# Kernel tuning notes

Measured on AMD Instinct MI355X. Metric: run time of the kernel, lower is better.

Reference implementation:

```python
import jax, jax.numpy as jnp
import numpy as np

B, S, DIM, BITS, HEXPERTS = 4, 4096, 2048, 32, 4


def setup_inputs() -> dict:
    key = jax.random.key(0)
    ks = jax.random.split(key, 6)
    scale = 1.0 / np.sqrt(DIM)
    return {
        "x": jax.random.normal(ks[0], (B, S, DIM), dtype=jnp.float32),
        "A1_w": jax.random.normal(ks[1], (BITS, DIM), dtype=jnp.float32) * scale,
        "A1_b": jax.random.normal(ks[2], (BITS,), dtype=jnp.float32) * 0.01,
        "emb": jax.random.normal(ks[3], (BITS, DIM), dtype=jnp.float32),
        "aggr_w": jax.random.normal(ks[4], (HEXPERTS,), dtype=jnp.float32) * 0.5,
        "aggr_b": jax.random.normal(ks[5], (1,), dtype=jnp.float32) * 0.01,
    }


def reference(x, A1_w, A1_b, emb, aggr_w, aggr_b):
    # Router: small linear [B,S,DIM] -> [B,S,BITS], softmax over bits.
    logits = jnp.einsum("bsd,kd->bsk", x, A1_w) + A1_b
    h_c = jax.nn.softmax(logits, axis=-1)
    # Top-k expert selection (k = Hexperts = 4), sorted descending like torch.topk.
    v, i = jax.lax.top_k(h_c, HEXPERTS)  # v,i: [B,S,4]
    # Gather expert embeddings: [B,S,4,DIM]
    h_emb = emb[i]
    # Scale by gate values and combine across experts with the 4->1 linear.
    # expert_aggr(h_emb.transpose(-2,-1)) == sum_e v[...,e]*h_emb[...,e,:]*w[e] + b
    out = jnp.einsum("bse,bsed,e->bsd", v, h_emb, aggr_w) + aggr_b[0]
    # Residual multiply (dropout p=0 -> identity).
    return x * out
```

## Files before the change

kernel.cpp:

```cpp
#include <hip/hip_runtime.h>


#define NTOK 16384
#define DIMV 2048

__global__ __launch_bounds__(512, 4) void fused_moe(
    const float* __restrict__ x,
    const float* __restrict__ A1w,
    const float* __restrict__ A1b,
    const float* __restrict__ emb,
    const float* __restrict__ aggw,
    const float* __restrict__ aggb,
    float* __restrict__ out)
{
    __shared__ float smem[9216];
    __shared__ float g_lds[256];

    const int tid  = threadIdx.x;
    const int wid  = tid >> 6;
    const int lane = tid & 63;
    const int tg   = lane & 7;
    const int kg   = lane >> 3;
    const int tok0 = blockIdx.x << 5;
    const int d0   = wid << 8;

    float* xs  = smem + wid * 1152;
    float* wsx = xs + 576;

    const int srow = lane >> 2;
    const int scol = (lane & 3) << 2;

    const float* xg0 = x   + (size_t)(tok0 + srow)      * DIMV + d0 + scol;
    const float* xg1 = x   + (size_t)(tok0 + srow + 16) * DIMV + d0 + scol;
    const float* wg0 = A1w + (size_t)(srow)             * DIMV + d0 + scol;
    const float* wg1 = A1w + (size_t)(srow + 16)        * DIMV + d0 + scol;

    float2 acc[4][4];
    #pragma unroll
    for (int i = 0; i < 4; ++i)
        #pragma unroll
        for (int j = 0; j < 4; ++j) acc[i][j] = make_float2(0.f, 0.f);

    float4 px0 = *(const float4*)(xg0);
    float4 px1 = *(const float4*)(xg1);
    float4 pw0 = *(const float4*)(wg0);
    float4 pw1 = *(const float4*)(wg1);

    for (int c = 0; c < 16; ++c) {
        {
            float* a = xs  + srow * 18 + scol;
            float* b = xs  + (srow + 16) * 18 + scol;
            float* d = wsx + srow * 18 + scol;
            float* e = wsx + (srow + 16) * 18 + scol;
            *(float2*)(a)     = make_float2(px0.x, px0.y);
            *(float2*)(a + 2) = make_float2(px0.z, px0.w);
            *(float2*)(b)     = make_float2(px1.x, px1.y);
            *(float2*)(b + 2) = make_float2(px1.z, px1.w);
            *(float2*)(d)     = make_float2(pw0.x, pw0.y);
            *(float2*)(d + 2) = make_float2(pw0.z, pw0.w);
            *(float2*)(e)     = make_float2(pw1.x, pw1.y);
            *(float2*)(e + 2) = make_float2(pw1.z, pw1.w);
        }
        {
            const int cn = (c + 1) & 15;
            px0 = *(const float4*)(xg0 + cn * 16);
            px1 = *(const float4*)(xg1 + cn * 16);
            pw0 = *(const float4*)(wg0 + cn * 16);
            pw1 = *(const float4*)(wg1 + cn * 16);
        }
        #pragma unroll
        for (int dd = 0; dd < 16; dd += 2) {
            float2 xv[4], wv[4];
            #pragma unroll
            for (int i = 0; i < 4; ++i)
                xv[i] = *(const float2*)&xs[(4 * tg + i) * 18 + dd];
            #pragma unroll
            for (int j = 0; j < 4; ++j)
                wv[j] = *(const float2*)&wsx[(4 * kg + j) * 18 + dd];
            #pragma unroll
            for (int i = 0; i < 4; ++i)
                #pragma unroll
                for (int j = 0; j < 4; ++j) {
                    acc[i][j].x = fmaf(xv[i].x, wv[j].x, acc[i][j].x);
                    acc[i][j].y = fmaf(xv[i].y, wv[j].y, acc[i][j].y);
                }
        }
    }

    __syncthreads();
    float* red = smem;
    #pragma unroll
    for (int i = 0; i < 4; ++i)
        #pragma unroll
        for (int j = 0; j < 4; ++j)
            red[(4 * tg + i) * 260 + ((4 * kg + j) << 3) + wid] =
                acc[i][j].x + acc[i][j].y;
    __syncthreads();

    if (tid < 32) {
        const int t = tid;
        float l[32];
        #pragma unroll
        for (int k = 0; k < 32; ++k) {
            float4 p0 = *(const float4*)&red[t * 260 + (k << 3)];
            float4 p1 = *(const float4*)&red[t * 260 + (k << 3) + 4];
            l[k] = ((p0.x + p0.y) + (p0.z + p0.w))
                 + ((p1.x + p1.y) + (p1.z + p1.w)) + A1b[k];
        }
        float m = l[0];
        #pragma unroll
        for (int k = 1; k < 32; ++k) m = fmaxf(m, l[k]);
        float s = 0.f;
        #pragma unroll
        for (int k = 0; k < 32; ++k) { l[k] = expf(l[k] - m); s += l[k]; }
        const float inv = 1.0f / s;

        unsigned used = 0u;
        #pragma unroll
        for (int e = 0; e < 4; ++e) {
            float best = -1.f; int bi = 0;
            #pragma unroll
            for (int k = 0; k < 32; ++k) {
                bool ok = !((used >> k) & 1u) && (l[k] > best);
                best = ok ? l[k] : best;
                bi   = ok ? k    : bi;
            }
            used |= (1u << bi);
            g_lds[t * 8 + e]     = best * inv * aggw[e];
            g_lds[t * 8 + 4 + e] = __uint_as_float((unsigned)bi);
        }
    }
    __syncthreads();

    const int tt  = tid >> 4;
    const int l16 = tid & 15;
    const float4 g = *(const float4*)&g_lds[tt * 8];
    const unsigned i0 = __float_as_uint(g_lds[tt * 8 + 4]);
    const unsigned i1 = __float_as_uint(g_lds[tt * 8 + 5]);
    const unsigned i2 = __float_as_uint(g_lds[tt * 8 + 6]);
    const unsigned i3 = __float_as_uint(g_lds[tt * 8 + 7]);
    const float bb = aggb[0];
    const size_t base = (size_t)(tok0 + tt) * DIMV;

    #pragma unroll 4
    for (int it = 0; it < 32; ++it) {
        const int d = (l16 << 2) + (it << 6);
        const float4 xv = *(const float4*)&x[base + d];
        const float4 e0 = *(const float4*)&emb[(size_t)i0 * DIMV + d];
        const float4 e1 = *(const float4*)&emb[(size_t)i1 * DIMV + d];
        const float4 e2 = *(const float4*)&emb[(size_t)i2 * DIMV + d];
        const float4 e3 = *(const float4*)&emb[(size_t)i3 * DIMV + d];
        float4 a, o;
        a.x = fmaf(g.x, e0.x, fmaf(g.y, e1.x, fmaf(g.z, e2.x, fmaf(g.w, e3.x, bb))));
        a.y = fmaf(g.x, e0.y, fmaf(g.y, e1.y, fmaf(g.z, e2.y, fmaf(g.w, e3.y, bb))));
        a.z = fmaf(g.x, e0.z, fmaf(g.y, e1.z, fmaf(g.z, e2.z, fmaf(g.w, e3.z, bb))));
        a.w = fmaf(g.x, e0.w, fmaf(g.y, e1.w, fmaf(g.z, e2.w, fmaf(g.w, e3.w, bb))));
        o.x = xv.x * a.x; o.y = xv.y * a.y; o.z = xv.z * a.z; o.w = xv.w * a.w;
        *(float4*)&out[base + d] = o;
    }
}

extern "C" void kernel_launch(void* const* d_in, const int* in_sizes, int n_in,
                              void* d_out, int out_size, void* d_ws, size_t ws_size,
                              hipStream_t stream)
{
    (void)in_sizes; (void)n_in; (void)out_size; (void)d_ws; (void)ws_size;
    const float* x    = (const float*)d_in[0];
    const float* A1w  = (const float*)d_in[1];
    const float* A1b  = (const float*)d_in[2];
    const float* emb  = (const float*)d_in[3];
    const float* aggw = (const float*)d_in[4];
    const float* aggb = (const float*)d_in[5];
    float* out = (float*)d_out;

    fused_moe<<<NTOK / 32, 512, 0, stream>>>(x, A1w, A1b, emb, aggw, aggb, out);
}
```

Baseline: 107.6 us.

## Restructure router GEMV: x in registers, A1w double-buffered via global_load_lds

Rewrites the router logit computation. Each lane now keeps x values for two tokens in registers and accumulates all 32 logits, while the A1w tile is streamed into LDS with a double-buffered direct global-to-LDS load. Partial sums are reduced with wave shuffles and then across four d-quarter waves in LDS, which removes the per-chunk staging of x into LDS. The cost is 64 accumulators per thread, which raises register pressure, a larger LDS footprint (64KB), and a full vmcnt wait every chunk.

Result: slower. 191.9 us (+78.2%).

```diff
diff --git a/kernel.cpp b/kernel.cpp
--- a/kernel.cpp
+++ b/kernel.cpp
@@ -3,6 +3,9 @@
 
 #define NTOK 16384
 #define DIMV 2048
+
+typedef const __attribute__((address_space(1))) unsigned int* as1_u32p;
+typedef __attribute__((address_space(3))) unsigned int* as3_u32p;
 
 __global__ __launch_bounds__(512, 4) void fused_moe(
     const float* __restrict__ x,
@@ -13,100 +16,103 @@
     const float* __restrict__ aggb,
     float* __restrict__ out)
 {
-    __shared__ float smem[9216];
-    __shared__ float g_lds[256];
+    __shared__ float smem[16384];
 
     const int tid  = threadIdx.x;
     const int wid  = tid >> 6;
     const int lane = tid & 63;
-    const int tg   = lane & 7;
-    const int kg   = lane >> 3;
+    const int g    = wid & 1;
+    const int q    = wid >> 1;
+    const int tg   = lane >> 3;
+    const int dpos = lane & 7;
     const int tok0 = blockIdx.x << 5;
-    const int d0   = wid << 8;
 
-    float* xs  = smem + wid * 1152;
-    float* wsx = xs + 576;
+    const int t0 = (g << 4) + tg;
+    const int t1 = t0 + 8;
+    const size_t xrow0 = (size_t)(tok0 + t0) * DIMV;
+    const size_t xrow1 = (size_t)(tok0 + t1) * DIMV;
+    const int dbase = (q << 9) + (dpos << 2);
 
-    const int srow = lane >> 2;
-    const int scol = (lane & 3) << 2;
+    float* wbuf = smem + (wid << 11);
 
-    const float* xg0 = x   + (size_t)(tok0 + srow)      * DIMV + d0 + scol;
-    const float* xg1 = x   + (size_t)(tok0 + srow + 16) * DIMV + d0 + scol;
-    const float* wg0 = A1w + (size_t)(srow)             * DIMV + d0 + scol;
-    const float* wg1 = A1w + (size_t)(srow + 16)        * DIMV + d0 + scol;
+    float acc0[32], acc1[32];
+    #pragma unroll
+    for (int k = 0; k < 32; ++k) { acc0[k] = 0.f; acc1[k] = 0.f; }
 
-    float2 acc[4][4];
-    #pragma unroll
-    for (int i = 0; i < 4; ++i)
+    const int wrow = lane >> 3;
+    const int wcol = (lane & 7) << 2;
+    const float* wsrc_base = A1w + (size_t)wrow * DIMV + (q << 9) + wcol;
+
+    {
+        float* ldst = wbuf;
         #pragma unroll
-        for (int j = 0; j < 4; ++j) acc[i][j] = make_float2(0.f, 0.f);
+        for (int j = 0; j < 4; ++j)
+            __builtin_amdgcn_global_load_lds(
+                (as1_u32p)(const void*)(wsrc_base + (size_t)(j << 3) * DIMV),
+                (as3_u32p)(void*)(ldst + (j << 8)), 16, 0, 0);
+    }
+    float4 xc0 = *(const float4*)&x[xrow0 + dbase];
+    float4 xc1 = *(const float4*)&x[xrow1 + dbase];
+    asm volatile("s_waitcnt vmcnt(0)" ::: "memory");
 
-    float4 px0 = *(const float4*)(xg0);
-    float4 px1 = *(const float4*)(xg1);
-    float4 pw0 = *(const float4*)(wg0);
-    float4 pw1 = *(const float4*)(wg1);
-
+    int cur = 0;
     for (int c = 0; c < 16; ++c) {
+        const int cn = (c < 15) ? (c + 1) : 15;
         {
-            float* a = xs  + srow * 18 + scol;
-            float* b = xs  + (srow + 16) * 18 + scol;
-            float* d = wsx + srow * 18 + scol;
-            float* e = wsx + (srow + 16) * 18 + scol;
-            *(float2*)(a)     = make_float2(px0.x, px0.y);
-            *(float2*)(a + 2) = make_float2(px0.z, px0.w);
-            *(float2*)(b)     = make_float2(px1.x, px1.y);
-            *(float2*)(b + 2) = make_float2(px1.z, px1.w);
-            *(float2*)(d)     = make_float2(pw0.x, pw0.y);
-            *(float2*)(d + 2) = make_float2(pw0.z, pw0.w);
-            *(float2*)(e)     = make_float2(pw1.x, pw1.y);
-            *(float2*)(e + 2) = make_float2(pw1.z, pw1.w);
-        }
-        {
-            const int cn = (c + 1) & 15;
-            px0 = *(const float4*)(xg0 + cn * 16);
-            px1 = *(const float4*)(xg1 + cn * 16);
-            pw0 = *(const float4*)(wg0 + cn * 16);
-            pw1 = *(const float4*)(wg1 + cn * 16);
-        }
-        #pragma unroll
-        for (int dd = 0; dd < 16; dd += 2) {
-            float2 xv[4], wv[4];
-            #pragma unroll
-            for (int i = 0; i < 4; ++i)
-                xv[i] = *(const float2*)&xs[(4 * tg + i) * 18 + dd];
+            const float* wsrc = wsrc_base + (cn << 5);
+            float* ldst = wbuf + ((cur ^ 1) << 10);
             #pragma unroll
             for (int j = 0; j < 4; ++j)
-                wv[j] = *(const float2*)&wsx[(4 * kg + j) * 18 + dd];
-            #pragma unroll
-            for (int i = 0; i < 4; ++i)
-                #pragma unroll
-                for (int j = 0; j < 4; ++j) {
-                    acc[i][j].x = fmaf(xv[i].x, wv[j].x, acc[i][j].x);
-                    acc[i][j].y = fmaf(xv[i].y, wv[j].y, acc[i][j].y);
-                }
+                __builtin_amdgcn_global_load_lds(
+                    (as1_u32p)(const void*)(wsrc + (size_t)(j << 3) * DIMV),
+                    (as3_u32p)(void*)(ldst + (j << 8)), 16, 0, 0);
         }
+        float4 xn0 = *(const float4*)&x[xrow0 + dbase + (cn << 5)];
+        float4 xn1 = *(const float4*)&x[xrow1 + dbase + (cn << 5)];
+        const float* wb = wbuf + (cur << 10);
+        #pragma unroll
+        for (int k = 0; k < 32; ++k) {
+            const float4 wv = *(const float4*)&wb[(k << 5) + (dpos << 2)];
+            acc0[k] = fmaf(xc0.w, wv.w, fmaf(xc0.z, wv.z,
+                      fmaf(xc0.y, wv.y, fmaf(xc0.x, wv.x, acc0[k]))));
+            acc1[k] = fmaf(xc1.w, wv.w, fmaf(xc1.z, wv.z,
+                      fmaf(xc1.y, wv.y, fmaf(xc1.x, wv.x, acc1[k]))));
+        }
+        asm volatile("s_waitcnt vmcnt(0)" ::: "memory");
+        xc0 = xn0; xc1 = xn1; cur ^= 1;
+    }
+
+    #pragma unroll
+    for (int k = 0; k < 32; ++k) {
+        float a = acc0[k], b = acc1[k];
+        a += __shfl_xor(a, 1); a += __shfl_xor(a, 2); a += __shfl_xor(a, 4);
+        b += __shfl_xor(b, 1); b += __shfl_xor(b, 2); b += __shfl_xor(b, 4);
+        acc0[k] = a; acc1[k] = b;
     }
 
     __syncthreads();
-    float* red = smem;
-    #pragma unroll
-    for (int i = 0; i < 4; ++i)
+    if (dpos == 0) {
+        float* r0 = smem + q * 1152 + t0 * 36;
+        float* r1 = smem + q * 1152 + t1 * 36;
         #pragma unroll
-        for (int j = 0; j < 4; ++j)
-            red[(4 * tg + i) * 260 + ((4 * kg + j) << 3) + wid] =
-                acc[i][j].x + acc[i][j].y;
+        for (int j = 0; j < 8; ++j) {
+            *(float4*)&r0[j << 2] = make_float4(acc0[4*j], acc0[4*j+1],
+                                                acc0[4*j+2], acc0[4*j+3]);
+            *(float4*)&r1[j << 2] = make_float4(acc1[4*j], acc1[4*j+1],
+                                                acc1[4*j+2], acc1[4*j+3]);
+        }
+    }
     __syncthreads();
 
+    float* gates = smem + 4608;
     if (tid < 32) {
         const int t = tid;
         float l[32];
         #pragma unroll
-        for (int k = 0; k < 32; ++k) {
-            float4 p0 = *(const float4*)&red[t * 260 + (k << 3)];
-            float4 p1 = *(const float4*)&red[t * 260 + (k << 3) + 4];
-            l[k] = ((p0.x + p0.y) + (p0.z + p0.w))
-                 + ((p1.x + p1.y) + (p1.z + p1.w)) + A1b[k];
-        }
+        for (int k = 0; k < 32; ++k)
+            l[k] = (smem[0    + t * 36 + k] + smem[1152 + t * 36 + k])
+                 + (smem[2304 + t * 36 + k] + smem[3456 + t * 36 + k])
+                 + A1b[k];
         float m = l[0];
         #pragma unroll
         for (int k = 1; k < 32; ++k) m = fmaxf(m, l[k]);
@@ -126,19 +132,19 @@
                 bi   = ok ? k    : bi;
             }
             used |= (1u << bi);
-            g_lds[t * 8 + e]     = best * inv * aggw[e];
-            g_lds[t * 8 + 4 + e] = __uint_as_float((unsigned)bi);
+            gates[t * 8 + e]     = best * inv * aggw[e];
+            gates[t * 8 + 4 + e] = __uint_as_float((unsigned)bi);
         }
     }
     __syncthreads();
 
     const int tt  = tid >> 4;
     const int l16 = tid & 15;
-    const float4 g = *(const float4*)&g_lds[tt * 8];
-    const unsigned i0 = __float_as_uint(g_lds[tt * 8 + 4]);
-    const unsigned i1 = __float_as_uint(g_lds[tt * 8 + 5]);
-    const unsigned i2 = __float_as_uint(g_lds[tt * 8 + 6]);
-    const unsigned i3 = __float_as_uint(g_lds[tt * 8 + 7]);
+    const float4 gv = *(const float4*)&gates[tt * 8];
+    const unsigned i0 = __float_as_uint(gates[tt * 8 + 4]);
+    const unsigned i1 = __float_as_uint(gates[tt * 8 + 5]);
+    const unsigned i2 = __float_as_uint(gates[tt * 8 + 6]);
+    const unsigned i3 = __float_as_uint(gates[tt * 8 + 7]);
     const float bb = aggb[0];
     const size_t base = (size_t)(tok0 + tt) * DIMV;
 
@@ -151,10 +157,10 @@
         const float4 e2 = *(const float4*)&emb[(size_t)i2 * DIMV + d];
         const float4 e3 = *(const float4*)&emb[(size_t)i3 * DIMV + d];
         float4 a, o;
-        a.x = fmaf(g.x, e0.x, fmaf(g.y, e1.x, fmaf(g.z, e2.x, fmaf(g.w, e3.x, bb))));
-        a.y = fmaf(g.x, e0.y, fmaf(g.y, e1.y, fmaf(g.z, e2.y, fmaf(g.w, e3.y, bb))));
-        a.z = fmaf(g.x, e0.z, fmaf(g.y, e1.z, fmaf(g.z, e2.z, fmaf(g.w, e3.z, bb))));
-        a.w = fmaf(g.x, e0.w, fmaf(g.y, e1.w, fmaf(g.z, e2.w, fmaf(g.w, e3.w, bb))));
+        a.x = fmaf(gv.x, e0.x, fmaf(gv.y, e1.x, fmaf(gv.z, e2.x, fmaf(gv.w, e3.x, bb))));
+        a.y = fmaf(gv.x, e0.y, fmaf(gv.y, e1.y, fmaf(gv.z, e2.y, fmaf(gv.w, e3.y, bb))));
+        a.z = fmaf(gv.x, e0.z, fmaf(gv.y, e1.z, fmaf(gv.z, e2.z, fmaf(gv.w, e3.z, bb))));
+        a.w = fmaf(gv.x, e0.w, fmaf(gv.y, e1.w, fmaf(gv.z, e2.w, fmaf(gv.w, e3.w, bb))));
         o.x = xv.x * a.x; o.y = xv.y * a.y; o.z = xv.z * a.z; o.w = xv.w * a.w;
         *(float4*)&out[base + d] = o;
     }
```
